# Kernel optimization log

Hardware: AMD Instinct MI355X
Metric: run time of the kernel (lower is better)

Reference implementation:

```python
import jax, jax.numpy as jnp
import numpy as np

STATE_DIM, ACTION_DIM, HIDDEN_DIM = 512, 64, 2048
INPUT_DIM = STATE_DIM + ACTION_DIM + 1  # 577
BATCH = 4096


def setup_inputs() -> dict:
    key = jax.random.key(0)
    ks = jax.random.split(key, 12)
    sc_x = 1.0 / np.sqrt(INPUT_DIM)
    sc_h = 1.0 / np.sqrt(HIDDEN_DIM)
    return {
        "s": jax.random.normal(ks[0], (BATCH, STATE_DIM), jnp.float32),
        "a_prev": jax.random.normal(ks[1], (BATCH, ACTION_DIM), jnp.float32),
        "r_prev": jax.random.normal(ks[2], (BATCH, 1), jnp.float32),
        "h": jnp.zeros((HIDDEN_DIM,), jnp.float32),
        "c": jnp.zeros((HIDDEN_DIM,), jnp.float32),
        # Fused gate weights: columns ordered [i, f, g(c-tilde), o]
        "Wx": jax.random.uniform(ks[3], (INPUT_DIM, 4 * HIDDEN_DIM), jnp.float32, -sc_x, sc_x),
        "Wh": jax.random.uniform(ks[4], (HIDDEN_DIM, 4 * HIDDEN_DIM), jnp.float32, -sc_h, sc_h),
        "bh": jax.random.uniform(ks[5], (4 * HIDDEN_DIM,), jnp.float32, -sc_h, sc_h),
        "Wa": jax.random.uniform(ks[6], (HIDDEN_DIM, ACTION_DIM), jnp.float32, -sc_h, sc_h),
        "ba": jax.random.uniform(ks[7], (ACTION_DIM,), jnp.float32, -sc_h, sc_h),
        "Wv": jax.random.uniform(ks[8], (HIDDEN_DIM, 1), jnp.float32, -sc_h, sc_h),
        "bv": jax.random.uniform(ks[9], (1,), jnp.float32, -sc_h, sc_h),
    }


def reference(s, a_prev, r_prev, h, c, Wx, Wh, bh, Wa, ba, Wv, bv):
    # x: [B, input_dim]
    x = jnp.concatenate([s, a_prev, r_prev], axis=1)
    # Two fused GEMMs replace the 8 separate small linears (same math).
    z = x @ Wx + h @ Wh + bh          # [B, 4H]
    zi, zf, zg, zo = jnp.split(z, 4, axis=-1)
    i = jax.nn.sigmoid(zi)
    f = jax.nn.sigmoid(zf)
    c_new = f * c + i * jnp.tanh(zg)  # [B, H] (c broadcast over batch)
    o = jax.nn.sigmoid(zo)
    h_new = o * jnp.tanh(c_new)       # [B, H]
    probs = jax.nn.softmax(h_new @ Wa + ba, axis=1)  # [B, A]
    v = h_new @ Wv + bv               # [B, 1]
    return (probs, v)
```

## Files before the change

### kernel.cpp

```cpp
#include <hip/hip_runtime.h>
#include <hip/hip_bf16.h>

#define BATCH   4096
#define SDIM    512
#define ADIM    64
#define IDIM    577
#define KP2     640
#define NKT2    10
#define HDIM    2048
#define ZDIM    8192

typedef __attribute__((ext_vector_type(8))) __bf16 bf16x8;
typedef __attribute__((ext_vector_type(4))) float  accx4;

__global__ __launch_bounds__(256) void setup_kernel(
    const float* __restrict__ s, const float* __restrict__ a_prev,
    const float* __restrict__ r_prev, const float* __restrict__ h,
    const float* __restrict__ wx, const float* __restrict__ wh,
    const float* __restrict__ wa,
    __hip_bfloat16* __restrict__ xb, __hip_bfloat16* __restrict__ wxt,
    __hip_bfloat16* __restrict__ waT, float* __restrict__ zh_w)
{
    __shared__ float stile[64 * 33];
    const int bid = blockIdx.x;
    const int t = threadIdx.x;

    if (bid < 2560) {
        const int kt2 = bid >> 8;
        const int nt  = bid & 255;
        const int c  = t & 31, r0 = t >> 5;
#pragma unroll
        for (int i = 0; i < 8; ++i) {
            int r = r0 + i * 8;
            int k = kt2 * 64 + r;
            stile[r * 33 + c] =
                (k < IDIM) ? wx[(size_t)k * ZDIM + nt * 32 + c] : 0.0f;
        }
        __syncthreads();
        const int nr = t >> 3, ch = t & 7;
        bf16x8 w8;
#pragma unroll
        for (int j = 0; j < 8; ++j)
            w8[j] = (__bf16)stile[(ch * 8 + j) * 33 + nr];
        *(bf16x8*)(wxt + (size_t)(nt * 32 + nr) * KP2 + kt2 * 64 + ch * 8) = w8;
    } else if (bid < 2816) {
        const int zb = bid - 2560;
        const int nb = zb & 31, ky = zb >> 5;
        const int n  = nb * 256 + t;
        const float* hp  = h + ky * 256;
        const float* whp = wh + (size_t)ky * 256 * ZDIM + n;
        float p = 0.0f;
#pragma unroll 8
        for (int kk = 0; kk < 256; ++kk)
            p = fmaf(hp[kk], whp[(size_t)kk * ZDIM], p);
        zh_w[ky * ZDIM + n] = p;
    } else if (bid < 6912) {
        const int row = bid - 2816;
        const float* srow = s + (size_t)row * SDIM;
        const float* arow = a_prev + (size_t)row * ADIM;
        __hip_bfloat16* xrow = xb + (size_t)row * KP2;
        for (int c = t; c < KP2; c += 256) {
            float v;
            if (c < SDIM)        v = srow[c];
            else if (c < 576)    v = arow[c - SDIM];
            else if (c == 576)   v = r_prev[row];
            else                 v = 0.0f;
            xrow[c] = __float2bfloat16(v);
        }
    } else {
        const int wb = bid - 6912;
        const int kt = wb >> 1, at = wb & 1;
        const int c  = t & 31, r0 = t >> 5;
#pragma unroll
        for (int i = 0; i < 4; ++i) {
            int r = r0 + i * 8;
            stile[r * 33 + c] = wa[(size_t)(kt * 32 + r) * ADIM + at * 32 + c];
        }
        __syncthreads();
#pragma unroll
        for (int i = 0; i < 4; ++i) {
            int r = r0 + i * 8;
            waT[(size_t)(at * 32 + r) * HDIM + kt * 32 + c] =
                __float2bfloat16(stile[c * 33 + r]);
        }
    }
}

__device__ __forceinline__ float sigmoid_f(float x) {
    return 1.0f / (1.0f + __expf(-x));
}
__device__ __forceinline__ float tanh_f(float x) {
    return 1.0f - 2.0f / (1.0f + __expf(2.0f * x));
}

__global__ __launch_bounds__(256) void lstm_gemm(
    const __hip_bfloat16* __restrict__ xb,
    const __hip_bfloat16* __restrict__ wxt,
    const float* __restrict__ zh_w,
    const float* __restrict__ bh,
    const float* __restrict__ cvec,
    __hip_bfloat16* __restrict__ hout)
{
    __shared__ __bf16 smA[128 * 64];
    __shared__ __bf16 smB[128 * 64];
    const int t    = threadIdx.x;
    const int lane = t & 63;
    const int wid  = t >> 6;
    const int m0   = blockIdx.x * 128;
    const int n0   = blockIdx.y * 32;

    accx4 acc[4][4] = {};

    const int srow = lane >> 3;
    const int slot = lane & 7;
    const int wm = wid >> 1, wn = wid & 1;
    const int fl15 = lane & 15;
    const int fhi  = lane >> 4;

    for (int kt = 0; kt < NKT2; ++kt) {
        __syncthreads();
#pragma unroll
        for (int i = 0; i < 4; ++i) {
            const int r = wid * 32 + i * 8 + srow;
            const int c = slot ^ (r & 7);
            const __hip_bfloat16* ga =
                xb + (size_t)(m0 + r) * KP2 + kt * 64 + c * 8;
            __bf16* la = smA + (wid * 32 + i * 8) * 64;
            __builtin_amdgcn_global_load_lds(
                (const __attribute__((address_space(1))) void*)ga,
                (__attribute__((address_space(3))) void*)la, 16, 0, 0);
            const int g = r >> 5, nn = r & 31;
            const __hip_bfloat16* gb =
                wxt + (size_t)(g * HDIM + n0 + nn) * KP2 + kt * 64 + c * 8;
            __bf16* lb = smB + (wid * 32 + i * 8) * 64;
            __builtin_amdgcn_global_load_lds(
                (const __attribute__((address_space(1))) void*)gb,
                (__attribute__((address_space(3))) void*)lb, 16, 0, 0);
        }
        __syncthreads();

#pragma unroll
        for (int hf = 0; hf < 2; ++hf) {
            const int ck = hf * 4 + fhi;
            const int sl = (ck ^ (lane & 7)) * 8;
            bf16x8 af[4], bfr[4];
#pragma unroll
            for (int rt = 0; rt < 4; ++rt)
                af[rt] = *(const bf16x8*)(smA +
                    (wm * 64 + rt * 16 + fl15) * 64 + sl);
#pragma unroll
            for (int g = 0; g < 4; ++g)
                bfr[g] = *(const bf16x8*)(smB +
                    (g * 32 + wn * 16 + fl15) * 64 + sl);
#pragma unroll
            for (int g = 0; g < 4; ++g)
#pragma unroll
                for (int rt = 0; rt < 4; ++rt)
                    acc[g][rt] = __builtin_amdgcn_mfma_f32_16x16x32_bf16(
                        af[rt], bfr[g], acc[g][rt], 0, 0, 0);
        }
    }

    const int colg = n0 + wn * 16 + fl15;
    float zsum[4];
#pragma unroll
    for (int g = 0; g < 4; ++g) {
        float v = bh[g * HDIM + colg];
#pragma unroll
        for (int j = 0; j < 8; ++j)
            v += zh_w[j * ZDIM + g * HDIM + colg];
        zsum[g] = v;
    }
    const float cv = cvec[colg];
#pragma unroll
    for (int rt = 0; rt < 4; ++rt) {
#pragma unroll
        for (int r = 0; r < 4; ++r) {
            const int row = m0 + wm * 64 + rt * 16 + (fhi << 2) + r;
            const float zi = acc[0][rt][r] + zsum[0];
            const float zf = acc[1][rt][r] + zsum[1];
            const float zg = acc[2][rt][r] + zsum[2];
            const float zo = acc[3][rt][r] + zsum[3];
            const float cn = sigmoid_f(zf) * cv + sigmoid_f(zi) * tanh_f(zg);
            const float hn = sigmoid_f(zo) * tanh_f(cn);
            hout[(size_t)row * HDIM + colg] = __float2bfloat16(hn);
        }
    }
}

__global__ __launch_bounds__(512) void head_kernel(
    const __hip_bfloat16* __restrict__ hnew,
    const __hip_bfloat16* __restrict__ waT,
    const float* __restrict__ wv,
    const float* __restrict__ ba, const float* __restrict__ bv,
    float* __restrict__ probs, float* __restrict__ vout)
{
    __shared__ float lg[2][16][68];
    __shared__ float vpart[2][16];
    const int t    = threadIdx.x;
    const int lane = t & 63;
    const int wid  = t >> 6;
    const int kh   = wid >> 2;
    const int wid2 = wid & 3;
    const int r0   = blockIdx.x * 16;
    const int fl15 = lane & 15, fhi = lane >> 4;

    const __bf16* arow = (const __bf16*)hnew +
        (size_t)(r0 + fl15) * HDIM + kh * 1024 + fhi * 8;
    const __bf16* brow = (const __bf16*)waT +
        (size_t)(wid2 * 16 + fl15) * HDIM + kh * 1024 + fhi * 8;
    const float* wvp = wv + kh * 1024 + fhi * 8;
    const bool do_v = (wid2 == 0);

    accx4 acc0 = {}, acc1 = {};
    float vacc = 0.0f;
#pragma unroll 4
    for (int kk = 0; kk < 1024; kk += 64) {
        bf16x8 a0 = *(const bf16x8*)(arow + kk);
        bf16x8 b0 = *(const bf16x8*)(brow + kk);
        bf16x8 a1 = *(const bf16x8*)(arow + kk + 32);
        bf16x8 b1 = *(const bf16x8*)(brow + kk + 32);
        acc0 = __builtin_amdgcn_mfma_f32_16x16x32_bf16(a0, b0, acc0, 0, 0, 0);
        acc1 = __builtin_amdgcn_mfma_f32_16x16x32_bf16(a1, b1, acc1, 0, 0, 0);
        if (do_v) {
#pragma unroll
            for (int j = 0; j < 8; ++j) {
                vacc = fmaf((float)a0[j], wvp[kk + j], vacc);
                vacc = fmaf((float)a1[j], wvp[kk + 32 + j], vacc);
            }
        }
    }
#pragma unroll
    for (int r = 0; r < 4; ++r)
        lg[kh][fhi * 4 + r][wid2 * 16 + fl15] = acc0[r] + acc1[r];
    if (do_v) {
        vacc += __shfl_xor(vacc, 16);
        vacc += __shfl_xor(vacc, 32);
        if (lane < 16) vpart[kh][lane] = vacc;
    }
    __syncthreads();

    const float bav = ba[lane];
#pragma unroll
    for (int i = 0; i < 2; ++i) {
        const int row = wid * 2 + i;
        const float logit = lg[0][row][lane] + lg[1][row][lane] + bav;
        float m = logit;
#pragma unroll
        for (int mask = 32; mask >= 1; mask >>= 1)
            m = fmaxf(m, __shfl_xor(m, mask));
        const float e = __expf(logit - m);
        float ssum = e;
#pragma unroll
        for (int mask = 32; mask >= 1; mask >>= 1)
            ssum += __shfl_xor(ssum, mask);
        probs[(size_t)(r0 + row) * 64 + lane] = e / ssum;
    }
    if (t < 16) vout[r0 + t] = vpart[0][t] + vpart[1][t] + bv[0];
}

extern "C" void kernel_launch(void* const* d_in, const int* in_sizes, int n_in,
                              void* d_out, int out_size, void* d_ws,
                              size_t ws_size, hipStream_t stream)
{
    const float* s      = (const float*)d_in[0];
    const float* a_prev = (const float*)d_in[1];
    const float* r_prev = (const float*)d_in[2];
    const float* h      = (const float*)d_in[3];
    const float* c      = (const float*)d_in[4];
    const float* Wx     = (const float*)d_in[5];
    const float* Wh     = (const float*)d_in[6];
    const float* bh     = (const float*)d_in[7];
    const float* Wa     = (const float*)d_in[8];
    const float* ba     = (const float*)d_in[9];
    const float* Wv     = (const float*)d_in[10];
    const float* bv     = (const float*)d_in[11];

    float* out   = (float*)d_out;
    float* probs = out;
    float* vout  = out + (size_t)BATCH * ADIM;

    char* ws = (char*)d_ws;
    __hip_bfloat16* xb   = (__hip_bfloat16*)ws;
    __hip_bfloat16* wxt  = (__hip_bfloat16*)(ws + 5242880);
    __hip_bfloat16* waT  = (__hip_bfloat16*)(ws + 15728640);
    float* zh_w          = (float*)(ws + 15990784);
    __hip_bfloat16* hnew = (__hip_bfloat16*)(ws + 16252928);

    setup_kernel<<<7040, 256, 0, stream>>>(
        s, a_prev, r_prev, h, Wx, Wh, Wa, xb, wxt, waT, zh_w);
    lstm_gemm<<<dim3(BATCH / 128, HDIM / 32), 256, 0, stream>>>(
        xb, wxt, zh_w, bh, c, hnew);
    head_kernel<<<BATCH / 16, 512, 0, stream>>>(
        hnew, waT, Wv, ba, bv, probs, vout);
}
```

Baseline: 235.8 us.

## Drop LDS staging in LSTM GEMM, widen N tile, split h@Wh finer

The LSTM gate GEMM no longer stages A and B tiles through shared memory. Each wave now loads its MFMA fragments straight from global memory (relying on L1/L2 reuse), and the N tile per block doubles to 64 columns with launch_bounds(256,2). The aim is to remove LDS round-trips and __syncthreads barriers. The risk is uncoalesced 16-byte strided global loads, and the 32 accumulator tiles per thread raise register pressure. The h@Wh partial-sum kernel also splits K into 16 chunks instead of 8, giving more blocks, and the epilogue sums the 16 partials.

After: 287.7 us. 1.22x slower.

```diff
diff --git a/kernel.cpp b/kernel.cpp
--- a/kernel.cpp
+++ b/kernel.cpp
@@ -43,19 +43,19 @@
         for (int j = 0; j < 8; ++j)
             w8[j] = (__bf16)stile[(ch * 8 + j) * 33 + nr];
         *(bf16x8*)(wxt + (size_t)(nt * 32 + nr) * KP2 + kt2 * 64 + ch * 8) = w8;
-    } else if (bid < 2816) {
+    } else if (bid < 3072) {
         const int zb = bid - 2560;
         const int nb = zb & 31, ky = zb >> 5;
         const int n  = nb * 256 + t;
-        const float* hp  = h + ky * 256;
-        const float* whp = wh + (size_t)ky * 256 * ZDIM + n;
+        const float* hp  = h + ky * 128;
+        const float* whp = wh + (size_t)ky * 128 * ZDIM + n;
         float p = 0.0f;
-#pragma unroll 8
-        for (int kk = 0; kk < 256; ++kk)
+#pragma unroll 32
+        for (int kk = 0; kk < 128; ++kk)
             p = fmaf(hp[kk], whp[(size_t)kk * ZDIM], p);
         zh_w[ky * ZDIM + n] = p;
-    } else if (bid < 6912) {
-        const int row = bid - 2816;
+    } else if (bid < 7168) {
+        const int row = bid - 3072;
         const float* srow = s + (size_t)row * SDIM;
         const float* arow = a_prev + (size_t)row * ADIM;
         __hip_bfloat16* xrow = xb + (size_t)row * KP2;
@@ -68,7 +68,7 @@
             xrow[c] = __float2bfloat16(v);
         }
     } else {
-        const int wb = bid - 6912;
+        const int wb = bid - 7168;
         const int kt = wb >> 1, at = wb & 1;
         const int c  = t & 31, r0 = t >> 5;
 #pragma unroll
@@ -93,7 +93,7 @@
     return 1.0f - 2.0f / (1.0f + __expf(2.0f * x));
 }
 
-__global__ __launch_bounds__(256) void lstm_gemm(
+__global__ __launch_bounds__(256, 2) void lstm_gemm(
     const __hip_bfloat16* __restrict__ xb,
     const __hip_bfloat16* __restrict__ wxt,
     const float* __restrict__ zh_w,
@@ -101,89 +101,70 @@
     const float* __restrict__ cvec,
     __hip_bfloat16* __restrict__ hout)
 {
-    __shared__ __bf16 smA[128 * 64];
-    __shared__ __bf16 smB[128 * 64];
     const int t    = threadIdx.x;
     const int lane = t & 63;
     const int wid  = t >> 6;
     const int m0   = blockIdx.x * 128;
-    const int n0   = blockIdx.y * 32;
-
-    accx4 acc[4][4] = {};
-
-    const int srow = lane >> 3;
-    const int slot = lane & 7;
-    const int wm = wid >> 1, wn = wid & 1;
+    const int n0   = blockIdx.y * 64;
+    const int wm   = wid >> 1, wn = wid & 1;
     const int fl15 = lane & 15;
     const int fhi  = lane >> 4;
 
-    for (int kt = 0; kt < NKT2; ++kt) {
-        __syncthreads();
-#pragma unroll
-        for (int i = 0; i < 4; ++i) {
-            const int r = wid * 32 + i * 8 + srow;
-            const int c = slot ^ (r & 7);
-            const __hip_bfloat16* ga =
-                xb + (size_t)(m0 + r) * KP2 + kt * 64 + c * 8;
-            __bf16* la = smA + (wid * 32 + i * 8) * 64;
-            __builtin_amdgcn_global_load_lds(
-                (const __attribute__((address_space(1))) void*)ga,
-                (__attribute__((address_space(3))) void*)la, 16, 0, 0);
-            const int g = r >> 5, nn = r & 31;
-            const __hip_bfloat16* gb =
-                wxt + (size_t)(g * HDIM + n0 + nn) * KP2 + kt * 64 + c * 8;
-            __bf16* lb = smB + (wid * 32 + i * 8) * 64;
-            __builtin_amdgcn_global_load_lds(
-                (const __attribute__((address_space(1))) void*)gb,
-                (__attribute__((address_space(3))) void*)lb, 16, 0, 0);
-        }
-        __syncthreads();
-
-#pragma unroll
-        for (int hf = 0; hf < 2; ++hf) {
-            const int ck = hf * 4 + fhi;
-            const int sl = (ck ^ (lane & 7)) * 8;
-            bf16x8 af[4], bfr[4];
-#pragma unroll
-            for (int rt = 0; rt < 4; ++rt)
-                af[rt] = *(const bf16x8*)(smA +
-                    (wm * 64 + rt * 16 + fl15) * 64 + sl);
-#pragma unroll
-            for (int g = 0; g < 4; ++g)
-                bfr[g] = *(const bf16x8*)(smB +
-                    (g * 32 + wn * 16 + fl15) * 64 + sl);
-#pragma unroll
-            for (int g = 0; g < 4; ++g)
+    accx4 acc[4][2][4] = {};
+
+    const __bf16* arow = (const __bf16*)xb +
+        (size_t)(m0 + wm * 64 + fl15) * KP2 + fhi * 8;
+    const __bf16* brow = (const __bf16*)wxt +
+        (size_t)(n0 + wn * 32 + fl15) * KP2 + fhi * 8;
+
+#pragma unroll 2
+    for (int ks = 0; ks < 2 * NKT2; ++ks) {
+        const int ko = ks * 32;
+        bf16x8 af[4];
+#pragma unroll
+        for (int rt = 0; rt < 4; ++rt)
+            af[rt] = *(const bf16x8*)(arow + (size_t)rt * 16 * KP2 + ko);
+#pragma unroll
+        for (int g = 0; g < 4; ++g) {
+#pragma unroll
+            for (int ht = 0; ht < 2; ++ht) {
+                bf16x8 bf = *(const bf16x8*)(brow +
+                    (size_t)(g * HDIM + ht * 16) * KP2 + ko);
 #pragma unroll
                 for (int rt = 0; rt < 4; ++rt)
-                    acc[g][rt] = __builtin_amdgcn_mfma_f32_16x16x32_bf16(
-                        af[rt], bfr[g], acc[g][rt], 0, 0, 0);
-        }
-    }
-
-    const int colg = n0 + wn * 16 + fl15;
-    float zsum[4];
-#pragma unroll
-    for (int g = 0; g < 4; ++g) {
-        float v = bh[g * HDIM + colg];
-#pragma unroll
-        for (int j = 0; j < 8; ++j)
-            v += zh_w[j * ZDIM + g * HDIM + colg];
-        zsum[g] = v;
-    }
-    const float cv = cvec[colg];
-#pragma unroll
-    for (int rt = 0; rt < 4; ++rt) {
-#pragma unroll
-        for (int r = 0; r < 4; ++r) {
-            const int row = m0 + wm * 64 + rt * 16 + (fhi << 2) + r;
-            const float zi = acc[0][rt][r] + zsum[0];
-            const float zf = acc[1][rt][r] + zsum[1];
-            const float zg = acc[2][rt][r] + zsum[2];
-            const float zo = acc[3][rt][r] + zsum[3];
-            const float cn = sigmoid_f(zf) * cv + sigmoid_f(zi) * tanh_f(zg);
-            const float hn = sigmoid_f(zo) * tanh_f(cn);
-            hout[(size_t)row * HDIM + colg] = __float2bfloat16(hn);
+                    acc[g][ht][rt] = __builtin_amdgcn_mfma_f32_16x16x32_bf16(
+                        af[rt], bf, acc[g][ht][rt], 0, 0, 0);
+            }
+        }
+    }
+
+#pragma unroll
+    for (int ht = 0; ht < 2; ++ht) {
+        const int colg = n0 + wn * 32 + ht * 16 + fl15;
+        float zsum[4];
+#pragma unroll
+        for (int g = 0; g < 4; ++g) {
+            float z = bh[g * HDIM + colg];
+#pragma unroll
+            for (int j = 0; j < 16; ++j)
+                z += zh_w[j * ZDIM + g * HDIM + colg];
+            zsum[g] = z;
+        }
+        const float cv = cvec[colg];
+#pragma unroll
+        for (int rt = 0; rt < 4; ++rt) {
+#pragma unroll
+            for (int r = 0; r < 4; ++r) {
+                const int row = m0 + wm * 64 + rt * 16 + (fhi << 2) + r;
+                const float zi = acc[0][ht][rt][r] + zsum[0];
+                const float zf = acc[1][ht][rt][r] + zsum[1];
+                const float zg = acc[2][ht][rt][r] + zsum[2];
+                const float zo = acc[3][ht][rt][r] + zsum[3];
+                const float cn = sigmoid_f(zf) * cv
+                               + sigmoid_f(zi) * tanh_f(zg);
+                const float hn = sigmoid_f(zo) * tanh_f(cn);
+                hout[(size_t)row * HDIM + colg] = __float2bfloat16(hn);
+            }
         }
     }
 }
@@ -285,11 +266,11 @@
     __hip_bfloat16* wxt  = (__hip_bfloat16*)(ws + 5242880);
     __hip_bfloat16* waT  = (__hip_bfloat16*)(ws + 15728640);
     float* zh_w          = (float*)(ws + 15990784);
-    __hip_bfloat16* hnew = (__hip_bfloat16*)(ws + 16252928);
-
-    setup_kernel<<<7040, 256, 0, stream>>>(
+    __hip_bfloat16* hnew = (__hip_bfloat16*)(ws + 16515072);
+
+    setup_kernel<<<7296, 256, 0, stream>>>(
         s, a_prev, r_prev, h, Wx, Wh, Wa, xb, wxt, waT, zh_w);
-    lstm_gemm<<<dim3(BATCH / 128, HDIM / 32), 256, 0, stream>>>(
+    lstm_gemm<<<dim3(BATCH / 128, HDIM / 64), 256, 0, stream>>>(
         xb, wxt, zh_w, bh, c, hnew);
     head_kernel<<<BATCH / 16, 512, 0, stream>>>(
         hnew, waT, Wv, ba, bv, probs, vout);
```

## Double-buffer LDS tiles in LSTM gate GEMM to overlap loads with MFMA

Applied to the files above, without the earlier changes.

Splits the LDS A/B tiles into two buffers so that the async global-to-LDS load of the next K tile is issued before computing on the current one, and drops one barrier per iteration. Global and LDS addresses are precomputed outside the loop. It also raises the unroll of the h@Wh reduction loop and adds a min-blocks-per-CU hint to launch bounds. LDS use doubles to 64KB per block, which may limit occupancy, and the launch-bounds hint may cause register pressure or spills.

New measurement: 231.7 us. About the same (-1.7%).

```diff
diff --git a/kernel.cpp b/kernel.cpp
--- a/kernel.cpp
+++ b/kernel.cpp
@@ -9,6 +9,7 @@
 #define NKT2    10
 #define HDIM    2048
 #define ZDIM    8192
+#define BUFE    (128 * 64)
 
 typedef __attribute__((ext_vector_type(8))) __bf16 bf16x8;
 typedef __attribute__((ext_vector_type(4))) float  accx4;
@@ -50,7 +51,7 @@
         const float* hp  = h + ky * 256;
         const float* whp = wh + (size_t)ky * 256 * ZDIM + n;
         float p = 0.0f;
-#pragma unroll 8
+#pragma unroll 16
         for (int kk = 0; kk < 256; ++kk)
             p = fmaf(hp[kk], whp[(size_t)kk * ZDIM], p);
         zh_w[ky * ZDIM + n] = p;
@@ -93,7 +94,7 @@
     return 1.0f - 2.0f / (1.0f + __expf(2.0f * x));
 }
 
-__global__ __launch_bounds__(256) void lstm_gemm(
+__global__ __launch_bounds__(256, 2) void lstm_gemm(
     const __hip_bfloat16* __restrict__ xb,
     const __hip_bfloat16* __restrict__ wxt,
     const float* __restrict__ zh_w,
@@ -101,56 +102,64 @@
     const float* __restrict__ cvec,
     __hip_bfloat16* __restrict__ hout)
 {
-    __shared__ __bf16 smA[128 * 64];
-    __shared__ __bf16 smB[128 * 64];
+    __shared__ __bf16 smA[2 * BUFE];
+    __shared__ __bf16 smB[2 * BUFE];
     const int t    = threadIdx.x;
     const int lane = t & 63;
     const int wid  = t >> 6;
     const int m0   = blockIdx.x * 128;
     const int n0   = blockIdx.y * 32;
+    const int wm   = wid >> 1, wn = wid & 1;
+    const int fl15 = lane & 15;
+    const int fhi  = lane >> 4;
 
     accx4 acc[4][4] = {};
 
     const int srow = lane >> 3;
     const int slot = lane & 7;
-    const int wm = wid >> 1, wn = wid & 1;
-    const int fl15 = lane & 15;
-    const int fhi  = lane >> 4;
-
-    for (int kt = 0; kt < NKT2; ++kt) {
-        __syncthreads();
+    const int cch  = slot ^ srow;
+    const __bf16* gA[4]; const __bf16* gB[4];
+    __bf16* lA[4]; __bf16* lB[4];
+#pragma unroll
+    for (int i = 0; i < 4; ++i) {
+        const int r = wid * 32 + i * 8 + srow;
+        gA[i] = (const __bf16*)xb + (size_t)(m0 + r) * KP2 + cch * 8;
+        const int g = r >> 5, nn = r & 31;
+        gB[i] = (const __bf16*)wxt +
+                (size_t)(g * HDIM + n0 + nn) * KP2 + cch * 8;
+        lA[i] = smA + (wid * 32 + i * 8) * 64;
+        lB[i] = smB + (wid * 32 + i * 8) * 64;
+    }
+
+    auto stage = [&](int tile, int p) {
+        const int ko = tile * 64;
+        const int po = p * BUFE;
 #pragma unroll
         for (int i = 0; i < 4; ++i) {
-            const int r = wid * 32 + i * 8 + srow;
-            const int c = slot ^ (r & 7);
-            const __hip_bfloat16* ga =
-                xb + (size_t)(m0 + r) * KP2 + kt * 64 + c * 8;
-            __bf16* la = smA + (wid * 32 + i * 8) * 64;
             __builtin_amdgcn_global_load_lds(
-                (const __attribute__((address_space(1))) void*)ga,
-                (__attribute__((address_space(3))) void*)la, 16, 0, 0);
-            const int g = r >> 5, nn = r & 31;
-            const __hip_bfloat16* gb =
-                wxt + (size_t)(g * HDIM + n0 + nn) * KP2 + kt * 64 + c * 8;
-            __bf16* lb = smB + (wid * 32 + i * 8) * 64;
+                (const __attribute__((address_space(1))) void*)(gA[i] + ko),
+                (__attribute__((address_space(3))) void*)(lA[i] + po),
+                16, 0, 0);
             __builtin_amdgcn_global_load_lds(
-                (const __attribute__((address_space(1))) void*)gb,
-                (__attribute__((address_space(3))) void*)lb, 16, 0, 0);
-        }
-        __syncthreads();
-
+                (const __attribute__((address_space(1))) void*)(gB[i] + ko),
+                (__attribute__((address_space(3))) void*)(lB[i] + po),
+                16, 0, 0);
+        }
+    };
+
+    auto compute = [&](int p) {
+        const int po = p * BUFE;
 #pragma unroll
         for (int hf = 0; hf < 2; ++hf) {
-            const int ck = hf * 4 + fhi;
-            const int sl = (ck ^ (lane & 7)) * 8;
+            const int sl = ((hf * 4 + fhi) ^ slot) * 8;
             bf16x8 af[4], bfr[4];
 #pragma unroll
             for (int rt = 0; rt < 4; ++rt)
-                af[rt] = *(const bf16x8*)(smA +
+                af[rt] = *(const bf16x8*)(smA + po +
                     (wm * 64 + rt * 16 + fl15) * 64 + sl);
 #pragma unroll
             for (int g = 0; g < 4; ++g)
-                bfr[g] = *(const bf16x8*)(smB +
+                bfr[g] = *(const bf16x8*)(smB + po +
                     (g * 32 + wn * 16 + fl15) * 64 + sl);
 #pragma unroll
             for (int g = 0; g < 4; ++g)
@@ -159,17 +168,27 @@
                     acc[g][rt] = __builtin_amdgcn_mfma_f32_16x16x32_bf16(
                         af[rt], bfr[g], acc[g][rt], 0, 0, 0);
         }
-    }
+    };
+
+    stage(0, 0);
+    __syncthreads();
+#pragma unroll
+    for (int kt = 0; kt < NKT2 - 1; ++kt) {
+        stage(kt + 1, (kt + 1) & 1);
+        compute(kt & 1);
+        __syncthreads();
+    }
+    compute((NKT2 - 1) & 1);
 
     const int colg = n0 + wn * 16 + fl15;
     float zsum[4];
 #pragma unroll
     for (int g = 0; g < 4; ++g) {
-        float v = bh[g * HDIM + colg];
+        float z = bh[g * HDIM + colg];
 #pragma unroll
         for (int j = 0; j < 8; ++j)
-            v += zh_w[j * ZDIM + g * HDIM + colg];
-        zsum[g] = v;
+            z += zh_w[j * ZDIM + g * HDIM + colg];
+        zsum[g] = z;
     }
     const float cv = cvec[colg];
 #pragma unroll
```
